# Performance work log

Measured on AMD Instinct MI355X. Metric: run time of the kernel, lower is better.

The kernel has to match this reference:

```python
import jax, jax.numpy as jnp
import numpy as np

B, GRID, CIN, COUT, TDIM, NMODES = 32, 128, 32, 32, 256, 32
M = NMODES // 2 + 1  # kept modes per axis = 17
FFT_NORM = 'forward'


def setup_inputs() -> dict:
    key = jax.random.key(0)
    ks = jax.random.split(key, 10)
    w_std = float(np.sqrt(1.0 / (2.0 * CIN)))          # normal_initializer(in_co_dim)
    k_std = float(np.sqrt(1.0 / TDIM))                 # ~lecun_normal for Dense kernels
    wshape = (M, M, CIN, COUT)
    return {
        'x': jax.random.normal(ks[0], (B, GRID, GRID, CIN), jnp.float32),
        't_emb': jax.random.normal(ks[1], (B, TDIM), jnp.float32),
        'w1_real': w_std * jax.random.normal(ks[2], wshape, jnp.float32),
        'w1_imag': w_std * jax.random.normal(ks[3], wshape, jnp.float32),
        'w2_real': w_std * jax.random.normal(ks[4], wshape, jnp.float32),
        'w2_imag': w_std * jax.random.normal(ks[5], wshape, jnp.float32),
        'k1_real': k_std * jax.random.normal(ks[6], (TDIM, M), jnp.float32),
        'k1_imag': k_std * jax.random.normal(ks[7], (TDIM, M), jnp.float32),
        'k2_real': k_std * jax.random.normal(ks[8], (TDIM, M), jnp.float32),
        'k2_imag': k_std * jax.random.normal(ks[9], (TDIM, M), jnp.float32),
    }


def reference(x, t_emb, w1_real, w1_imag, w2_real, w2_imag,
              k1_real, k1_imag, k2_real, k2_imag):
    b, n = x.shape[0], x.shape[1]
    # rFFT2 over spatial axes: (b, n, n//2+1, cin) complex
    x_ft = jnp.fft.rfft2(x, axes=(1, 2), norm=FFT_NORM)

    w1 = w1_real + 1j * w1_imag  # (M, M, cin, cout)
    w2 = w2_real + 1j * w2_imag
    # Time modulation: Dense(no bias) -> complex per-mode scale t[b, i].
    # The original builds diag(t) and einsums it into the weights; that equals a
    # simple broadcast scale over the first mode axis, fused here.
    t1 = (t_emb @ k1_real) + 1j * (t_emb @ k1_imag)  # (b, M)
    t2 = (t_emb @ k2_real) + 1j * (t_emb @ k2_imag)

    # Mode-truncated complex channel contraction, scaled by t along axis i.
    xf1 = jnp.einsum('bijc,ijco->bijo', x_ft[:, :M, :M, :], w1) * t1[:, :, None, None]
    xf2 = jnp.einsum('bijc,ijco->bijo', x_ft[:, -M:, :M, :], w2) * t2[:, :, None, None]

    out_ft = jnp.zeros((b, n, n // 2 + 1, COUT), dtype=jnp.complex64)
    out_ft = out_ft.at[:, :M, :M, :].set(xf1)
    out_ft = out_ft.at[:, -M:, :M, :].set(xf2)

    return jnp.fft.irfft2(out_ft, s=(n, n), axes=(1, 2), norm=FFT_NORM)
```

## Files before the change

### kernel.cpp

```cpp
#include <hip/hip_runtime.h>
#include <stdint.h>


#define TWO_PI_OVER_128 0.04908738521234052f

__device__ __forceinline__ float4 f4add(float4 a, float4 b) {
    return make_float4(a.x + b.x, a.y + b.y, a.z + b.z, a.w + b.w);
}
__device__ __forceinline__ float4 f4sub(float4 a, float4 b) {
    return make_float4(a.x - b.x, a.y - b.y, a.z - b.z, a.w - b.w);
}

__global__ __launch_bounds__(128) void k_tproj(
    const float* __restrict__ temb, const float* __restrict__ k1r, const float* __restrict__ k1i,
    const float* __restrict__ k2r, const float* __restrict__ k2i, float* __restrict__ tbuf)
{
    int b = blockIdx.x, tid = threadIdx.x;
    __shared__ float ts[256];
    for (int d = tid; d < 256; d += 128) ts[d] = temb[b * 256 + d];
    __syncthreads();
    if (tid < 68) {
        int which = (tid >= 34) ? 1 : 0;
        int rem = tid - which * 34;
        int i = rem >> 1, part = rem & 1;
        const float* kp = which ? (part ? k2i : k2r) : (part ? k1i : k1r);
        float a0 = 0.f, a1 = 0.f, a2 = 0.f, a3 = 0.f;
        for (int d = 0; d < 256; d += 4) {
            a0 = fmaf(ts[d],     kp[(d)     * 17 + i], a0);
            a1 = fmaf(ts[d + 1], kp[(d + 1) * 17 + i], a1);
            a2 = fmaf(ts[d + 2], kp[(d + 2) * 17 + i], a2);
            a3 = fmaf(ts[d + 3], kp[(d + 3) * 17 + i], a3);
        }
        tbuf[((which * 32 + b) * 17 + i) * 2 + part] = (a0 + a1) + (a2 + a3);
    }
}

__global__ __launch_bounds__(64) void k_fwd_y(const float* __restrict__ x, float2* __restrict__ T1)
{
    int blk = blockIdx.x;
    int b = blk >> 7, xr = blk & 127;
    __shared__ float xs[128 * 32];
    __shared__ float2 cst[128];
    int tid = threadIdx.x;
    {
        float s0, c0; sincosf(TWO_PI_OVER_128 * (float)tid, &s0, &c0);
        cst[tid] = make_float2(c0, -s0);
        float s1, c1; sincosf(TWO_PI_OVER_128 * (float)(tid + 64), &s1, &c1);
        cst[tid + 64] = make_float2(c1, -s1);
    }
    const float4* xv = (const float4*)(x + ((size_t)blk << 12));
    float4* xs4 = (float4*)xs;
#pragma unroll
    for (int i = 0; i < 16; ++i) xs4[tid + (i << 6)] = xv[tid + (i << 6)];
    __syncthreads();
    for (int i = tid; i < 1024; i += 64) {
        int c = i & 31, t = i >> 5;
        if (t < 31) {
            int y = t + 1;
            float a  = xs[(y << 5) + c],        bb = xs[((64 - y) << 5) + c];
            float cc = xs[((64 + y) << 5) + c], d  = xs[((128 - y) << 5) + c];
            float Sy = a + d, Dy = a - d, Sm = bb + cc, Dm = bb - cc;
            xs[(y << 5) + c]         = Sy + Sm;
            xs[((64 - y) << 5) + c]  = Sy - Sm;
            xs[((128 - y) << 5) + c] = Dy - Dm;
            xs[((64 + y) << 5) + c]  = Dy + Dm;
        } else {
            float a = xs[(32 << 5) + c], q = xs[(96 << 5) + c];
            xs[(32 << 5) + c] = a + q;
            xs[(96 << 5) + c] = a - q;
        }
    }
    __syncthreads();
    int jg = tid >> 3, cg = tid & 7, c0 = cg << 2;
    int p = jg & 1;
    float re[2][4] = {{0,0,0,0},{0,0,0,0}}, im[2][4] = {{0,0,0,0},{0,0,0,0}};
    int j0 = jg, j1 = jg + 8;
    int idx0 = 0, idx1 = 0;
    for (int y = 1; y <= 31; ++y) {
        idx0 = (idx0 + j0) & 127;
        idx1 = (idx1 + j1) & 127;
        float2 w0 = cst[idx0], w1 = cst[idx1];
        int sr = p ? (64 - y) : y;
        int dr = p ? (64 + y) : (128 - y);
        float4 s = *(const float4*)&xs[(sr << 5) + c0];
        float4 d = *(const float4*)&xs[(dr << 5) + c0];
        re[0][0] = fmaf(s.x, w0.x, re[0][0]);
        re[0][1] = fmaf(s.y, w0.x, re[0][1]);
        re[0][2] = fmaf(s.z, w0.x, re[0][2]);
        re[0][3] = fmaf(s.w, w0.x, re[0][3]);
        im[0][0] = fmaf(d.x, w0.y, im[0][0]);
        im[0][1] = fmaf(d.y, w0.y, im[0][1]);
        im[0][2] = fmaf(d.z, w0.y, im[0][2]);
        im[0][3] = fmaf(d.w, w0.y, im[0][3]);
        re[1][0] = fmaf(s.x, w1.x, re[1][0]);
        re[1][1] = fmaf(s.y, w1.x, re[1][1]);
        re[1][2] = fmaf(s.z, w1.x, re[1][2]);
        re[1][3] = fmaf(s.w, w1.x, re[1][3]);
        im[1][0] = fmaf(d.x, w1.y, im[1][0]);
        im[1][1] = fmaf(d.y, w1.y, im[1][1]);
        im[1][2] = fmaf(d.z, w1.y, im[1][2]);
        im[1][3] = fmaf(d.w, w1.y, im[1][3]);
    }
    const float s_ = 1.f / 16384.f;
    float x0[4], x64[4], S32v[4], D32v[4];
    *(float4*)x0   = *(const float4*)&xs[c0];
    *(float4*)x64  = *(const float4*)&xs[(64 << 5) + c0];
    *(float4*)S32v = *(const float4*)&xs[(32 << 5) + c0];
    *(float4*)D32v = *(const float4*)&xs[(96 << 5) + c0];
    float2 w32 = cst[(j0 << 5) & 127];
    float sg = p ? -1.f : 1.f;
#pragma unroll
    for (int t = 0; t < 2; ++t) {
        int j = jg + t * 8;
        float2* pp = T1 + (((size_t)(b * 17 + j) * 128 + xr) << 5) + c0;
        float4 v0 = make_float4((re[t][0] + x0[0] + sg * x64[0] + S32v[0] * w32.x) * s_,
                                (im[t][0] + D32v[0] * w32.y) * s_,
                                (re[t][1] + x0[1] + sg * x64[1] + S32v[1] * w32.x) * s_,
                                (im[t][1] + D32v[1] * w32.y) * s_);
        float4 v1 = make_float4((re[t][2] + x0[2] + sg * x64[2] + S32v[2] * w32.x) * s_,
                                (im[t][2] + D32v[2] * w32.y) * s_,
                                (re[t][3] + x0[3] + sg * x64[3] + S32v[3] * w32.x) * s_,
                                (im[t][3] + D32v[3] * w32.y) * s_);
        ((float4*)pp)[0] = v0; ((float4*)pp)[1] = v1;
    }
    {
        float re2[4] = {0,0,0,0}, im2[4] = {0,0,0,0};
        float2 w16 = cst[(16 * (jg + 1)) & 127];
        for (int y = jg + 1; y <= 31; y += 8) {
            float4 s = *(const float4*)&xs[(y << 5) + c0];
            float4 d = *(const float4*)&xs[((128 - y) << 5) + c0];
            re2[0] = fmaf(s.x, w16.x, re2[0]); re2[1] = fmaf(s.y, w16.x, re2[1]);
            re2[2] = fmaf(s.z, w16.x, re2[2]); re2[3] = fmaf(s.w, w16.x, re2[3]);
            im2[0] = fmaf(d.x, w16.y, im2[0]); im2[1] = fmaf(d.y, w16.y, im2[1]);
            im2[2] = fmaf(d.z, w16.y, im2[2]); im2[3] = fmaf(d.w, w16.y, im2[3]);
        }
#pragma unroll
        for (int t = 0; t < 4; ++t) {
            re2[t] += __shfl_xor(re2[t], 8);
            re2[t] += __shfl_xor(re2[t], 16);
            re2[t] += __shfl_xor(re2[t], 32);
            im2[t] += __shfl_xor(im2[t], 8);
            im2[t] += __shfl_xor(im2[t], 16);
            im2[t] += __shfl_xor(im2[t], 32);
        }
        if (jg == 0) {
            float2* pp = T1 + (((size_t)(b * 17 + 16) * 128 + xr) << 5) + c0;
            float4 v0 = make_float4((re2[0] + x0[0] + x64[0] + S32v[0]) * s_, im2[0] * s_,
                                    (re2[1] + x0[1] + x64[1] + S32v[1]) * s_, im2[1] * s_);
            float4 v1 = make_float4((re2[2] + x0[2] + x64[2] + S32v[2]) * s_, im2[2] * s_,
                                    (re2[3] + x0[3] + x64[3] + S32v[3]) * s_, im2[3] * s_);
            ((float4*)pp)[0] = v0; ((float4*)pp)[1] = v1;
        }
    }
}

#define XFS 34
__global__ __launch_bounds__(512) void k_mid_fused(
    const float2* __restrict__ T1, const float* __restrict__ w1r, const float* __restrict__ w1i,
    const float* __restrict__ w2r, const float* __restrict__ w2i,
    const float* __restrict__ temb, const float* __restrict__ k1r, const float* __restrict__ k1i,
    const float* __restrict__ k2r, const float* __restrict__ k2i, float2* __restrict__ U)
{
    int blk = blockIdx.x;
    int b = blk / 17, j = blk - b * 17;
    __shared__ float4 Ts4[2048];
    __shared__ float2 Xf[34 * XFS];
    __shared__ float2 cst[128];
    __shared__ float tl[68];
    int tid = threadIdx.x;
    const float4* s4 = (const float4*)(T1 + (size_t)blk * 4096);
    for (int i = tid; i < 2048; i += 512) Ts4[i] = s4[i];
    if (tid < 128) {
        float s, c; sincosf(TWO_PI_OVER_128 * (float)tid, &s, &c);
        cst[tid] = make_float2(c, s);
    }
    __syncthreads();
    {
        int t = tid >> 4, cp = tid & 15;
        if (t < 31) {
            int y = t + 1;
            float4 a  = Ts4[(y << 4) + cp],        bb = Ts4[((64 - y) << 4) + cp];
            float4 cc = Ts4[((64 + y) << 4) + cp], d  = Ts4[((128 - y) << 4) + cp];
            float4 Sy = f4add(a, d), Dy = f4sub(a, d);
            float4 Sm = f4add(bb, cc), Dm = f4sub(bb, cc);
            Ts4[(y << 4) + cp]         = f4add(Sy, Sm);
            Ts4[((64 - y) << 4) + cp]  = f4sub(Sy, Sm);
            Ts4[((128 - y) << 4) + cp] = f4sub(Dy, Dm);
            Ts4[((64 + y) << 4) + cp]  = f4add(Dy, Dm);
        } else {
            float4 a = Ts4[(32 << 4) + cp], q = Ts4[(96 << 4) + cp];
            Ts4[(32 << 4) + cp] = f4add(a, q);
            Ts4[(96 << 4) + cp] = f4sub(a, q);
        }
    }
    __syncthreads();
    if (tid < 288) {
        int cp = tid & 15, u = tid >> 4;
        int f = (u < 16) ? (u + 1) : ((u == 16) ? 0 : 111);
        int p = f & 1;
        float4 t0 = Ts4[cp], t64 = Ts4[(64 << 4) + cp];
        float P0=0,Q0=0,R0=0,T0=0,P1=0,Q1=0,R1=0,T1a=0;
        int idx = 0;
        for (int xx = 1; xx <= 31; ++xx) {
            idx = (idx + f) & 127;
            float2 w = cst[idx];
            float4 S = Ts4[((p ? (64 - xx) : xx) << 4) + cp];
            float4 D = Ts4[((p ? (64 + xx) : (128 - xx)) << 4) + cp];
            P0 = fmaf(S.x, w.x, P0); Q0 = fmaf(D.y, w.y, Q0);
            R0 = fmaf(S.y, w.x, R0); T0 = fmaf(D.x, w.y, T0);
            P1 = fmaf(S.z, w.x, P1); Q1 = fmaf(D.w, w.y, Q1);
            R1 = fmaf(S.w, w.x, R1); T1a = fmaf(D.z, w.y, T1a);
        }
        {
            float2 w32 = cst[(f << 5) & 127];
            float4 S32 = Ts4[(32 << 4) + cp], D32 = Ts4[(96 << 4) + cp];
            P0 = fmaf(S32.x, w32.x, P0); Q0 = fmaf(D32.y, w32.y, Q0);
            R0 = fmaf(S32.y, w32.x, R0); T0 = fmaf(D32.x, w32.y, T0);
            P1 = fmaf(S32.z, w32.x, P1); Q1 = fmaf(D32.w, w32.y, Q1);
            R1 = fmaf(S32.w, w32.x, R1); T1a = fmaf(D32.z, w32.y, T1a);
        }
        float sg = p ? -1.f : 1.f;
        float b0r = t0.x + sg * t64.x, b0i = t0.y + sg * t64.y;
        float b1r = t0.z + sg * t64.z, b1i = t0.w + sg * t64.w;
        int ia = (u == 16) ? 0 : ((u == 17) ? 17 : f);
        Xf[ia * XFS + cp*2]   = make_float2(P0 + Q0 + b0r, R0 - T0 + b0i);
        Xf[ia * XFS + cp*2+1] = make_float2(P1 + Q1 + b1r, R1 - T1a + b1i);
        if (u < 16) {
            int ib = 34 - f;
            Xf[ib * XFS + cp*2]   = make_float2(P0 - Q0 + b0r, R0 + T0 + b0i);
            Xf[ib * XFS + cp*2+1] = make_float2(P1 - Q1 + b1r, R1 + T1a + b1i);
        }
    } else if (tid >= 320 && tid < 388) {
        int r = tid - 320;
        int which = (r >= 34) ? 1 : 0;
        int rem = r - which * 34;
        int i = rem >> 1, part = rem & 1;
        const float* kp = which ? (part ? k2i : k2r) : (part ? k1i : k1r);
        const float* tb = temb + b * 256;
        float a0 = 0.f, a1 = 0.f, a2 = 0.f, a3 = 0.f;
        for (int d = 0; d < 256; d += 4) {
            a0 = fmaf(tb[d],     kp[(d)     * 17 + i], a0);
            a1 = fmaf(tb[d + 1], kp[(d + 1) * 17 + i], a1);
            a2 = fmaf(tb[d + 2], kp[(d + 2) * 17 + i], a2);
            a3 = fmaf(tb[d + 3], kp[(d + 3) * 17 + i], a3);
        }
        tl[which * 34 + (i << 1) + part] = (a0 + a1) + (a2 + a3);
    }
    __syncthreads();
    float2* Ys = (float2*)Ts4;
    if (tid < 272) {
        int oq = tid & 7, ii = tid >> 3;
        int o0 = oq << 2;
        int irow = (ii < 17) ? ii : ii - 17;
        const float* wr = ((ii < 17) ? w1r : w2r) + ((irow * 17 + j) << 10) + o0;
        const float* wi = ((ii < 17) ? w1i : w2i) + ((irow * 17 + j) << 10) + o0;
        float ar0=0,ai0=0,ar1=0,ai1=0,ar2=0,ai2=0,ar3=0,ai3=0;
#pragma unroll 4
        for (int c = 0; c < 32; ++c) {
            float2 xv = Xf[ii * XFS + c];
            float4 wre = *(const float4*)(wr + (c << 5));
            float4 wim = *(const float4*)(wi + (c << 5));
            ar0 = fmaf(xv.x, wre.x, ar0); ar0 = fmaf(-xv.y, wim.x, ar0);
            ai0 = fmaf(xv.x, wim.x, ai0); ai0 = fmaf( xv.y, wre.x, ai0);
            ar1 = fmaf(xv.x, wre.y, ar1); ar1 = fmaf(-xv.y, wim.y, ar1);
            ai1 = fmaf(xv.x, wim.y, ai1); ai1 = fmaf( xv.y, wre.y, ai1);
            ar2 = fmaf(xv.x, wre.z, ar2); ar2 = fmaf(-xv.y, wim.z, ar2);
            ai2 = fmaf(xv.x, wim.z, ai2); ai2 = fmaf( xv.y, wre.z, ai2);
            ar3 = fmaf(xv.x, wre.w, ar3); ar3 = fmaf(-xv.y, wim.w, ar3);
            ai3 = fmaf(xv.x, wim.w, ai3); ai3 = fmaf( xv.y, wre.w, ai3);
        }
        int which = (ii >= 17) ? 1 : 0;
        float tr = tl[which * 34 + (irow << 1)], ti = tl[which * 34 + (irow << 1) + 1];
        float2* yp = Ys + ii * 32 + o0;
        float4 y01 = make_float4(ar0 * tr - ai0 * ti, ar0 * ti + ai0 * tr,
                                 ar1 * tr - ai1 * ti, ar1 * ti + ai1 * tr);
        float4 y23 = make_float4(ar2 * tr - ai2 * ti, ar2 * ti + ai2 * tr,
                                 ar3 * tr - ai3 * ti, ar3 * ti + ai3 * tr);
        ((float4*)yp)[0] = y01;
        ((float4*)yp)[1] = y23;
    }
    __syncthreads();
    {
        int o = tid & 31, g = tid >> 5;
        float yr[34], yi[34];
#pragma unroll
        for (int i = 0; i < 34; ++i) { float2 v = Ys[i * 32 + o]; yr[i] = v.x; yi[i] = v.y; }
        float2* Ub = U + ((size_t)b * 128 * 17 + j) * 32 + o;
        if (g == 0) {
            float sr = 0.f, si = 0.f;
#pragma unroll
            for (int i = 0; i < 34; ++i) { sr += yr[i]; si += yi[i]; }
            Ub[0] = make_float2(sr, si);
        }
        if (g == 1) {
            float sr = 0.f, si = 0.f;
#pragma unroll
            for (int i = 0; i < 34; ++i) {
                float sg2 = (i & 1) ? -1.f : 1.f;
                sr = fmaf(sg2, yr[i], sr); si = fmaf(sg2, yi[i], si);
            }
            Ub[(size_t)64 * 544] = make_float2(sr, si);
        }
        for (int k = 0; k < 2; ++k) {
            int x = 1 + g + (k << 4);
            float A1e=0,A1o=0,A2e=0,A2o=0,A3e=0,A3o=0,A4e=0,A4o=0;
            int idx = 0;
#pragma unroll
            for (int i = 0; i < 17; ++i) {
                float2 w = cst[idx];
                if (i & 1) {
                    A1o = fmaf(yr[i], w.x, A1o); A4o = fmaf(yr[i], w.y, A4o);
                    A3o = fmaf(yi[i], w.x, A3o); A2o = fmaf(yi[i], w.y, A2o);
                } else {
                    A1e = fmaf(yr[i], w.x, A1e); A4e = fmaf(yr[i], w.y, A4e);
                    A3e = fmaf(yi[i], w.x, A3e); A2e = fmaf(yi[i], w.y, A2e);
                }
                idx = (idx + x) & 127;
            }
            idx = (111 * x) & 127;
#pragma unroll
            for (int i = 17; i < 34; ++i) {
                float2 w = cst[idx];
                if (i & 1) {
                    A1o = fmaf(yr[i], w.x, A1o); A4o = fmaf(yr[i], w.y, A4o);
                    A3o = fmaf(yi[i], w.x, A3o); A2o = fmaf(yi[i], w.y, A2o);
                } else {
                    A1e = fmaf(yr[i], w.x, A1e); A4e = fmaf(yr[i], w.y, A4e);
                    A3e = fmaf(yi[i], w.x, A3e); A2e = fmaf(yi[i], w.y, A2e);
                }
                idx = (idx + x) & 127;
            }
            float A1 = A1e + A1o, A2 = A2e + A2o, A3 = A3e + A3o, A4 = A4e + A4o;
            float E1 = A1e - A1o, E2 = A2o - A2e, E3 = A3e - A3o, E4 = A4o - A4e;
            Ub[(size_t)x * 544]         = make_float2(A1 - A2, A3 + A4);
            Ub[(size_t)(128 - x) * 544] = make_float2(A1 + A2, A3 - A4);
            Ub[(size_t)(64 - x) * 544]  = make_float2(E1 - E2, E3 + E4);
            Ub[(size_t)(64 + x) * 544]  = make_float2(E1 + E2, E3 - E4);
        }
    }
}

__global__ __launch_bounds__(256) void k_fwd_x_mix(
    const float2* __restrict__ T1, const float* __restrict__ w1r, const float* __restrict__ w1i,
    const float* __restrict__ w2r, const float* __restrict__ w2i,
    const float* __restrict__ tbuf, float2* __restrict__ Y)
{
    int blk = blockIdx.x;
    int b = blk / 17, j = blk - b * 17;
    __shared__ float4 Ts4[2048];
    __shared__ float2 Xf[34 * 32];
    int tid = threadIdx.x;
    const float4* s4 = (const float4*)(T1 + (size_t)blk * 4096);
    for (int i = tid; i < 2048; i += 256) Ts4[i] = s4[i];
    __syncthreads();
    {
        int cp = tid & 15, g = tid >> 4;
        int il[3] = {g, g + 16, g + 32};
        float stc[3], sts[3];
#pragma unroll
        for (int t = 0; t < 3; ++t) {
            int i = il[t];
            int f = (i < 17) ? i : i + 94;
            float a = -TWO_PI_OVER_128 * (float)(f & 127);
            sincosf(a, &sts[t], &stc[t]);
        }
        float cr[3] = {1.f, 1.f, 1.f}, ci[3] = {0.f, 0.f, 0.f};
        float r0[3] = {0,0,0}, i0[3] = {0,0,0}, r1[3] = {0,0,0}, i1[3] = {0,0,0};
        const float4* Tc = Ts4 + cp;
#pragma unroll 2
        for (int xx = 0; xx < 128; ++xx) {
            float4 tv = Tc[xx << 4];
#pragma unroll
            for (int t = 0; t < 3; ++t) {
                r0[t] += tv.x * cr[t] - tv.y * ci[t];
                i0[t] += tv.x * ci[t] + tv.y * cr[t];
                r1[t] += tv.z * cr[t] - tv.w * ci[t];
                i1[t] += tv.z * ci[t] + tv.w * cr[t];
                float nr = cr[t] * stc[t] - ci[t] * sts[t];
                ci[t] = fmaf(cr[t], sts[t], ci[t] * stc[t]);
                cr[t] = nr;
            }
        }
#pragma unroll
        for (int t = 0; t < 3; ++t) {
            int i = il[t];
            if (i < 34) {
                Xf[i * 32 + cp * 2]     = make_float2(r0[t], i0[t]);
// ... 76 lines not shown

__global__ __launch_bounds__(128) void k_inv_y(const float2* __restrict__ U, float* __restrict__ out)
{
    int blk = blockIdx.x;
    __shared__ float2 Us[17 * 32];
    __shared__ float2 cst[128];
    int tid = threadIdx.x;
    {
        float s, c; sincosf(TWO_PI_OVER_128 * (float)tid, &s, &c);
        cst[tid] = make_float2(c, s);
    }
    const float4* src4 = (const float4*)(U + (size_t)blk * 544);
    float4* Us4 = (float4*)Us;
    for (int i = tid; i < 272; i += 128) Us4[i] = src4[i];
    __syncthreads();
    int cg = tid & 15, yg = tid >> 4, c0 = cg << 1;
    float base0, base1;
    {
        float4 v = *(const float4*)&Us[c0];
        base0 = v.x; base1 = v.z;
    }
    float urr[16][2], uii[16][2];
#pragma unroll
    for (int jj = 1; jj <= 16; ++jj) {
        float4 v = *(const float4*)&Us[jj * 32 + c0];
        urr[jj-1][0] = 2.f * v.x; uii[jj-1][0] = 2.f * v.y;
        urr[jj-1][1] = 2.f * v.z; uii[jj-1][1] = 2.f * v.w;
    }
    float* op = out + ((size_t)blk << 12);
    for (int k = 0; k < 4; ++k) {
        int y = 1 + yg + (k << 3);
        float Ae0=0,Ao0=0,Be0=0,Bo0=0,Ae1=0,Ao1=0,Be1=0,Bo1=0;
        int idx = y;
#pragma unroll
        for (int jj = 0; jj < 16; ++jj) {
            float2 w = cst[idx];
            if (jj & 1) {
                Ae0 = fmaf(urr[jj][0], w.x, Ae0); Be0 = fmaf(uii[jj][0], w.y, Be0);
                Ae1 = fmaf(urr[jj][1], w.x, Ae1); Be1 = fmaf(uii[jj][1], w.y, Be1);
            } else {
                Ao0 = fmaf(urr[jj][0], w.x, Ao0); Bo0 = fmaf(uii[jj][0], w.y, Bo0);
                Ao1 = fmaf(urr[jj][1], w.x, Ao1); Bo1 = fmaf(uii[jj][1], w.y, Bo1);
            }
            idx = (idx + y) & 127;
        }
        float s0 = Ae0 + Ao0, d0 = Be0 + Bo0, e0 = Ae0 - Ao0, f0 = Be0 - Bo0;
        float s1 = Ae1 + Ao1, d1 = Be1 + Bo1, e1 = Ae1 - Ao1, f1 = Be1 - Bo1;
        *(float2*)&op[(y << 5) + c0]         = make_float2(base0 + s0 - d0, base1 + s1 - d1);
        *(float2*)&op[((128 - y) << 5) + c0] = make_float2(base0 + s0 + d0, base1 + s1 + d1);
        *(float2*)&op[((64 - y) << 5) + c0]  = make_float2(base0 + e0 + f0, base1 + e1 + f1);
        *(float2*)&op[((64 + y) << 5) + c0]  = make_float2(base0 + e0 - f0, base1 + e1 - f1);
    }
    if (yg == 0) {
        float s0 = 0.f, s1 = 0.f, a0 = 0.f, a1 = 0.f;
#pragma unroll
        for (int jj = 0; jj < 16; ++jj) {
            s0 += urr[jj][0]; s1 += urr[jj][1];
            float sg = (jj & 1) ? 1.f : -1.f;
            a0 = fmaf(sg, urr[jj][0], a0); a1 = fmaf(sg, urr[jj][1], a1);
        }
        *(float2*)&op[c0]             = make_float2(base0 + s0, base1 + s1);
        *(float2*)&op[(64 << 5) + c0] = make_float2(base0 + a0, base1 + a1);
    }
}

extern "C" void kernel_launch(void* const* d_in, const int* in_sizes, int n_in,
                              void* d_out, int out_size, void* d_ws, size_t ws_size,
                              hipStream_t stream)
{
    const float* x    = (const float*)d_in[0];
    const float* temb = (const float*)d_in[1];
    const float* w1r  = (const float*)d_in[2];
    const float* w1i  = (const float*)d_in[3];
    const float* w2r  = (const float*)d_in[4];
    const float* w2i  = (const float*)d_in[5];
    const float* k1r  = (const float*)d_in[6];
    const float* k1i  = (const float*)d_in[7];
    const float* k2r  = (const float*)d_in[8];
    const float* k2i  = (const float*)d_in[9];
    float* out = (float*)d_out;

    char* ws = (char*)d_ws;
    const size_t T1_BYTES = 17825792;
    const size_t NEED_FUSED = 2 * T1_BYTES + 8704;

    if (ws_size >= NEED_FUSED) {
        float2* T1 = (float2*)ws;
        float2* U  = (float2*)(ws + T1_BYTES);
        k_fwd_y    <<<4096, 64,  0, stream>>>(x, T1);
        k_mid_fused<<<544,  512, 0, stream>>>(T1, w1r, w1i, w2r, w2i,
                                              temb, k1r, k1i, k2r, k2i, U);
        k_inv_y    <<<4096, 128, 0, stream>>>(U, out);
    } else {
        float2* T1 = (float2*)ws;
        float2* Yb = (float2*)(ws + T1_BYTES);
        float*  tb = (float*)(ws + T1_BYTES + 4734976);
        float2* U  = T1;
        k_tproj    <<<32,   128, 0, stream>>>(temb, k1r, k1i, k2r, k2i, tb);
        k_fwd_y    <<<4096, 64,  0, stream>>>(x, T1);
        k_fwd_x_mix<<<544,  256, 0, stream>>>(T1, w1r, w1i, w2r, w2i, tb, Yb);
        k_inv_x    <<<544,  256, 0, stream>>>(Yb, U);
        k_inv_y    <<<4096, 128, 0, stream>>>(U, out);
    }
}
```

Baseline: 183.1 us.

## Split fused mid kernel into forward-x and mix/inverse-x kernels, drop LDS staging in fwd_y

k_fwd_y no longer stages each row in shared memory. It reads the four folded rows straight from global memory and applies the butterfly fold in registers, with two x-rows per 128-thread block. The former 544-block fused middle kernel becomes two kernels of 1088 blocks each: a forward x-DFT split by mode parity that writes truncated modes to a new global buffer and computes the time projection, then a channel mix plus inverse x-DFT split by output-channel half. This raises parallelism and lowers per-block shared memory. The cost is an extra launch, an extra global round trip for the truncated modes, and redundant global loads in fwd_y.

```diff
diff --git a/kernel.cpp b/kernel.cpp
--- a/kernel.cpp
+++ b/kernel.cpp
@@ -35,44 +35,23 @@
     }
 }
 
-__global__ __launch_bounds__(64) void k_fwd_y(const float* __restrict__ x, float2* __restrict__ T1)
+__global__ __launch_bounds__(128) void k_fwd_y(const float* __restrict__ x, float2* __restrict__ T1)
 {
     int blk = blockIdx.x;
-    int b = blk >> 7, xr = blk & 127;
-    __shared__ float xs[128 * 32];
     __shared__ float2 cst[128];
     int tid = threadIdx.x;
-    {
+    if (tid < 128) {
         float s0, c0; sincosf(TWO_PI_OVER_128 * (float)tid, &s0, &c0);
         cst[tid] = make_float2(c0, -s0);
-        float s1, c1; sincosf(TWO_PI_OVER_128 * (float)(tid + 64), &s1, &c1);
-        cst[tid + 64] = make_float2(c1, -s1);
-    }
-    const float4* xv = (const float4*)(x + ((size_t)blk << 12));
-    float4* xs4 = (float4*)xs;
-#pragma unroll
-    for (int i = 0; i < 16; ++i) xs4[tid + (i << 6)] = xv[tid + (i << 6)];
-    __syncthreads();
-    for (int i = tid; i < 1024; i += 64) {
-        int c = i & 31, t = i >> 5;
-        if (t < 31) {
-            int y = t + 1;
-            float a  = xs[(y << 5) + c],        bb = xs[((64 - y) << 5) + c];
-            float cc = xs[((64 + y) << 5) + c], d  = xs[((128 - y) << 5) + c];
-            float Sy = a + d, Dy = a - d, Sm = bb + cc, Dm = bb - cc;
-            xs[(y << 5) + c]         = Sy + Sm;
-            xs[((64 - y) << 5) + c]  = Sy - Sm;
-            xs[((128 - y) << 5) + c] = Dy - Dm;
-            xs[((64 + y) << 5) + c]  = Dy + Dm;
-        } else {
-            float a = xs[(32 << 5) + c], q = xs[(96 << 5) + c];
-            xs[(32 << 5) + c] = a + q;
-            xs[(96 << 5) + c] = a - q;
-        }
-    }
-    __syncthreads();
-    int jg = tid >> 3, cg = tid & 7, c0 = cg << 2;
+    }
+    __syncthreads();
+    int half = tid >> 6, t64i = tid & 63;
+    int b = blk >> 6, xp = blk & 63;
+    int xr = (xp << 1) + half;
+    const float* W = x + (((size_t)(b * 128 + xr)) << 12);
+    int jg = t64i >> 3, cg = t64i & 7, c0 = cg << 2;
     int p = jg & 1;
+    float sfold = p ? -1.f : 1.f;
     float re[2][4] = {{0,0,0,0},{0,0,0,0}}, im[2][4] = {{0,0,0,0},{0,0,0,0}};
     int j0 = jg, j1 = jg + 8;
     int idx0 = 0, idx1 = 0;
@@ -80,59 +59,71 @@
         idx0 = (idx0 + j0) & 127;
         idx1 = (idx1 + j1) & 127;
         float2 w0 = cst[idx0], w1 = cst[idx1];
-        int sr = p ? (64 - y) : y;
-        int dr = p ? (64 + y) : (128 - y);
-        float4 s = *(const float4*)&xs[(sr << 5) + c0];
-        float4 d = *(const float4*)&xs[(dr << 5) + c0];
+        float4 a  = *(const float4*)&W[(y << 5) + c0];
+        float4 d  = *(const float4*)&W[((128 - y) << 5) + c0];
+        float4 bb = *(const float4*)&W[((64 - y) << 5) + c0];
+        float4 cc = *(const float4*)&W[((64 + y) << 5) + c0];
+        float4 Sy = f4add(a, d), Dy = f4sub(a, d);
+        float4 Sm = f4add(bb, cc), Dm = f4sub(bb, cc);
+        float4 s = make_float4(fmaf(sfold, Sm.x, Sy.x), fmaf(sfold, Sm.y, Sy.y),
+                               fmaf(sfold, Sm.z, Sy.z), fmaf(sfold, Sm.w, Sy.w));
+        float4 dd = make_float4(fmaf(-sfold, Dm.x, Dy.x), fmaf(-sfold, Dm.y, Dy.y),
+                                fmaf(-sfold, Dm.z, Dy.z), fmaf(-sfold, Dm.w, Dy.w));
         re[0][0] = fmaf(s.x, w0.x, re[0][0]);
         re[0][1] = fmaf(s.y, w0.x, re[0][1]);
         re[0][2] = fmaf(s.z, w0.x, re[0][2]);
         re[0][3] = fmaf(s.w, w0.x, re[0][3]);
-        im[0][0] = fmaf(d.x, w0.y, im[0][0]);
-        im[0][1] = fmaf(d.y, w0.y, im[0][1]);
-        im[0][2] = fmaf(d.z, w0.y, im[0][2]);
-        im[0][3] = fmaf(d.w, w0.y, im[0][3]);
+        im[0][0] = fmaf(dd.x, w0.y, im[0][0]);
+        im[0][1] = fmaf(dd.y, w0.y, im[0][1]);
+        im[0][2] = fmaf(dd.z, w0.y, im[0][2]);
+        im[0][3] = fmaf(dd.w, w0.y, im[0][3]);
         re[1][0] = fmaf(s.x, w1.x, re[1][0]);
         re[1][1] = fmaf(s.y, w1.x, re[1][1]);
         re[1][2] = fmaf(s.z, w1.x, re[1][2]);
         re[1][3] = fmaf(s.w, w1.x, re[1][3]);
-        im[1][0] = fmaf(d.x, w1.y, im[1][0]);
-        im[1][1] = fmaf(d.y, w1.y, im[1][1]);
-        im[1][2] = fmaf(d.z, w1.y, im[1][2]);
-        im[1][3] = fmaf(d.w, w1.y, im[1][3]);
+        im[1][0] = fmaf(dd.x, w1.y, im[1][0]);
+        im[1][1] = fmaf(dd.y, w1.y, im[1][1]);
+        im[1][2] = fmaf(dd.z, w1.y, im[1][2]);
+        im[1][3] = fmaf(dd.w, w1.y, im[1][3]);
     }
     const float s_ = 1.f / 16384.f;
-    float x0[4], x64[4], S32v[4], D32v[4];
-    *(float4*)x0   = *(const float4*)&xs[c0];
-    *(float4*)x64  = *(const float4*)&xs[(64 << 5) + c0];
-    *(float4*)S32v = *(const float4*)&xs[(32 << 5) + c0];
-    *(float4*)D32v = *(const float4*)&xs[(96 << 5) + c0];
+    float4 x0  = *(const float4*)&W[c0];
+    float4 x64 = *(const float4*)&W[(64 << 5) + c0];
+    float4 r32 = *(const float4*)&W[(32 << 5) + c0];
+    float4 r96 = *(const float4*)&W[(96 << 5) + c0];
+    float4 S32 = f4add(r32, r96), D32 = f4sub(r32, r96);
     float2 w32 = cst[(j0 << 5) & 127];
+    float x0a[4], x64a[4], S32a[4], D32a[4];
+    *(float4*)x0a = x0; *(float4*)x64a = x64; *(float4*)S32a = S32; *(float4*)D32a = D32;
     float sg = p ? -1.f : 1.f;
 #pragma unroll
     for (int t = 0; t < 2; ++t) {
         int j = jg + t * 8;
         float2* pp = T1 + (((size_t)(b * 17 + j) * 128 + xr) << 5) + c0;
-        float4 v0 = make_float4((re[t][0] + x0[0] + sg * x64[0] + S32v[0] * w32.x) * s_,
-                                (im[t][0] + D32v[0] * w32.y) * s_,
-                                (re[t][1] + x0[1] + sg * x64[1] + S32v[1] * w32.x) * s_,
-                                (im[t][1] + D32v[1] * w32.y) * s_);
-        float4 v1 = make_float4((re[t][2] + x0[2] + sg * x64[2] + S32v[2] * w32.x) * s_,
-                                (im[t][2] + D32v[2] * w32.y) * s_,
-                                (re[t][3] + x0[3] + sg * x64[3] + S32v[3] * w32.x) * s_,
-                                (im[t][3] + D32v[3] * w32.y) * s_);
+        float4 v0 = make_float4((re[t][0] + x0a[0] + sg * x64a[0] + S32a[0] * w32.x) * s_,
+                                (im[t][0] + D32a[0] * w32.y) * s_,
+                                (re[t][1] + x0a[1] + sg * x64a[1] + S32a[1] * w32.x) * s_,
+                                (im[t][1] + D32a[1] * w32.y) * s_);
+        float4 v1 = make_float4((re[t][2] + x0a[2] + sg * x64a[2] + S32a[2] * w32.x) * s_,
+                                (im[t][2] + D32a[2] * w32.y) * s_,
+                                (re[t][3] + x0a[3] + sg * x64a[3] + S32a[3] * w32.x) * s_,
+                                (im[t][3] + D32a[3] * w32.y) * s_);
         ((float4*)pp)[0] = v0; ((float4*)pp)[1] = v1;
     }
     {
         float re2[4] = {0,0,0,0}, im2[4] = {0,0,0,0};
         float2 w16 = cst[(16 * (jg + 1)) & 127];
         for (int y = jg + 1; y <= 31; y += 8) {
-            float4 s = *(const float4*)&xs[(y << 5) + c0];
-            float4 d = *(const float4*)&xs[((128 - y) << 5) + c0];
+            float4 a  = *(const float4*)&W[(y << 5) + c0];
+            float4 d  = *(const float4*)&W[((128 - y) << 5) + c0];
+            float4 bb = *(const float4*)&W[((64 - y) << 5) + c0];
+            float4 cc = *(const float4*)&W[((64 + y) << 5) + c0];
+            float4 s  = f4add(f4add(a, d), f4add(bb, cc));
+            float4 dd = f4sub(f4sub(a, d), f4sub(bb, cc));
             re2[0] = fmaf(s.x, w16.x, re2[0]); re2[1] = fmaf(s.y, w16.x, re2[1]);
             re2[2] = fmaf(s.z, w16.x, re2[2]); re2[3] = fmaf(s.w, w16.x, re2[3]);
-            im2[0] = fmaf(d.x, w16.y, im2[0]); im2[1] = fmaf(d.y, w16.y, im2[1]);
-            im2[2] = fmaf(d.z, w16.y, im2[2]); im2[3] = fmaf(d.w, w16.y, im2[3]);
+            im2[0] = fmaf(dd.x, w16.y, im2[0]); im2[1] = fmaf(dd.y, w16.y, im2[1]);
+            im2[2] = fmaf(dd.z, w16.y, im2[2]); im2[3] = fmaf(dd.w, w16.y, im2[3]);
         }
 #pragma unroll
         for (int t = 0; t < 4; ++t) {
@@ -145,67 +136,70 @@
         }
         if (jg == 0) {
             float2* pp = T1 + (((size_t)(b * 17 + 16) * 128 + xr) << 5) + c0;
-            float4 v0 = make_float4((re2[0] + x0[0] + x64[0] + S32v[0]) * s_, im2[0] * s_,
-                                    (re2[1] + x0[1] + x64[1] + S32v[1]) * s_, im2[1] * s_);
-            float4 v1 = make_float4((re2[2] + x0[2] + x64[2] + S32v[2]) * s_, im2[2] * s_,
-                                    (re2[3] + x0[3] + x64[3] + S32v[3]) * s_, im2[3] * s_);
+            float4 v0 = make_float4((re2[0] + x0a[0] + x64a[0] + S32a[0]) * s_, im2[0] * s_,
+                                    (re2[1] + x0a[1] + x64a[1] + S32a[1]) * s_, im2[1] * s_);
+            float4 v1 = make_float4((re2[2] + x0a[2] + x64a[2] + S32a[2]) * s_, im2[2] * s_,
+                                    (re2[3] + x0a[3] + x64a[3] + S32a[3]) * s_, im2[3] * s_);
             ((float4*)pp)[0] = v0; ((float4*)pp)[1] = v1;
         }
     }
 }
 
-#define XFS 34
-__global__ __launch_bounds__(512) void k_mid_fused(
-    const float2* __restrict__ T1, const float* __restrict__ w1r, const float* __restrict__ w1i,
-    const float* __restrict__ w2r, const float* __restrict__ w2i,
-    const float* __restrict__ temb, const float* __restrict__ k1r, const float* __restrict__ k1i,
-    const float* __restrict__ k2r, const float* __restrict__ k2i, float2* __restrict__ U)
+__global__ __launch_bounds__(256) void k_fwd_x(
+    const float2* __restrict__ T1, const float* __restrict__ temb,
+    const float* __restrict__ k1r, const float* __restrict__ k1i,
+    const float* __restrict__ k2r, const float* __restrict__ k2i,
+    float2* __restrict__ Xfg, float* __restrict__ tbuf)
 {
     int blk = blockIdx.x;
-    int b = blk / 17, j = blk - b * 17;
-    __shared__ float4 Ts4[2048];
-    __shared__ float2 Xf[34 * XFS];
+    int b = blk / 34, r = blk - b * 34;
+    int j = r >> 1, par = r & 1;
+    __shared__ float4 FH[65 * 16];
     __shared__ float2 cst[128];
-    __shared__ float tl[68];
     int tid = threadIdx.x;
-    const float4* s4 = (const float4*)(T1 + (size_t)blk * 4096);
-    for (int i = tid; i < 2048; i += 512) Ts4[i] = s4[i];
     if (tid < 128) {
         float s, c; sincosf(TWO_PI_OVER_128 * (float)tid, &s, &c);
         cst[tid] = make_float2(c, s);
     }
-    __syncthreads();
-    {
-        int t = tid >> 4, cp = tid & 15;
-        if (t < 31) {
-            int y = t + 1;
-            float4 a  = Ts4[(y << 4) + cp],        bb = Ts4[((64 - y) << 4) + cp];
-            float4 cc = Ts4[((64 + y) << 4) + cp], d  = Ts4[((128 - y) << 4) + cp];
+    const float4* T = (const float4*)(T1 + (size_t)(b * 17 + j) * 4096);
+    float sfold = par ? -1.f : 1.f;
+    for (int i = tid; i < 544; i += 256) {
+        if (i < 496) {
+            int y = (i >> 4) + 1, cp = i & 15;
+            float4 a  = T[(y << 4) + cp];
+            float4 d  = T[((128 - y) << 4) + cp];
+            float4 bb = T[((64 - y) << 4) + cp];
+            float4 cc = T[((64 + y) << 4) + cp];
             float4 Sy = f4add(a, d), Dy = f4sub(a, d);
             float4 Sm = f4add(bb, cc), Dm = f4sub(bb, cc);
-            Ts4[(y << 4) + cp]         = f4add(Sy, Sm);
-            Ts4[((64 - y) << 4) + cp]  = f4sub(Sy, Sm);
-            Ts4[((128 - y) << 4) + cp] = f4sub(Dy, Dm);
-            Ts4[((64 + y) << 4) + cp]  = f4add(Dy, Dm);
+            FH[((y - 1) << 4) + cp] = make_float4(
+                fmaf(sfold, Sm.x, Sy.x), fmaf(sfold, Sm.y, Sy.y),
+                fmaf(sfold, Sm.z, Sy.z), fmaf(sfold, Sm.w, Sy.w));
+            FH[((30 + y) << 4) + cp] = make_float4(
+                fmaf(-sfold, Dm.x, Dy.x), fmaf(-sfold, Dm.y, Dy.y),
+                fmaf(-sfold, Dm.z, Dy.z), fmaf(-sfold, Dm.w, Dy.w));
+        } else if (i < 512) {
+            int cp = i - 496;
+            float4 s32 = T[(32 << 4) + cp], s96 = T[(96 << 4) + cp];
+            FH[(62 << 4) + cp] = par ? f4sub(s32, s96) : f4add(s32, s96);
         } else {
-            float4 a = Ts4[(32 << 4) + cp], q = Ts4[(96 << 4) + cp];
-            Ts4[(32 << 4) + cp] = f4add(a, q);
-            Ts4[(96 << 4) + cp] = f4sub(a, q);
-        }
-    }
-    __syncthreads();
-    if (tid < 288) {
+            int k = i - 512, cp = k & 15;
+            if (k < 16) FH[(63 << 4) + cp] = T[cp];
+            else        FH[(64 << 4) + cp] = T[(64 << 4) + cp];
+        }
+    }
+    __syncthreads();
+    if (tid < 144) {
         int cp = tid & 15, u = tid >> 4;
-        int f = (u < 16) ? (u + 1) : ((u == 16) ? 0 : 111);
-        int p = f & 1;
-        float4 t0 = Ts4[cp], t64 = Ts4[(64 << 4) + cp];
+        int f = par ? ((u < 8) ? (2 * u + 1) : 111)
+                    : ((u < 8) ? (2 * u + 2) : 0);
         float P0=0,Q0=0,R0=0,T0=0,P1=0,Q1=0,R1=0,T1a=0;
         int idx = 0;
         for (int xx = 1; xx <= 31; ++xx) {
             idx = (idx + f) & 127;
             float2 w = cst[idx];
-            float4 S = Ts4[((p ? (64 - xx) : xx) << 4) + cp];
-            float4 D = Ts4[((p ? (64 + xx) : (128 - xx)) << 4) + cp];
+            float4 S = FH[((xx - 1) << 4) + cp];
+            float4 D = FH[((30 + xx) << 4) + cp];
             P0 = fmaf(S.x, w.x, P0); Q0 = fmaf(D.y, w.y, Q0);
             R0 = fmaf(S.y, w.x, R0); T0 = fmaf(D.x, w.y, T0);
             P1 = fmaf(S.z, w.x, P1); Q1 = fmaf(D.w, w.y, Q1);
@@ -213,27 +207,34 @@
         }
         {
             float2 w32 = cst[(f << 5) & 127];
-            float4 S32 = Ts4[(32 << 4) + cp], D32 = Ts4[(96 << 4) + cp];
-            P0 = fmaf(S32.x, w32.x, P0); Q0 = fmaf(D32.y, w32.y, Q0);
-            R0 = fmaf(S32.y, w32.x, R0); T0 = fmaf(D32.x, w32.y, T0);
-            P1 = fmaf(S32.z, w32.x, P1); Q1 = fmaf(D32.w, w32.y, Q1);
-            R1 = fmaf(S32.w, w32.x, R1); T1a = fmaf(D32.z, w32.y, T1a);
-        }
-        float sg = p ? -1.f : 1.f;
+            float4 SD = FH[(62 << 4) + cp];
+            if (par == 0) {
+                P0 = fmaf(SD.x, w32.x, P0); R0 = fmaf(SD.y, w32.x, R0);
+                P1 = fmaf(SD.z, w32.x, P1); R1 = fmaf(SD.w, w32.x, R1);
+            } else {
+                Q0 = fmaf(SD.y, w32.y, Q0); T0 = fmaf(SD.x, w32.y, T0);
+                Q1 = fmaf(SD.w, w32.y, Q1); T1a = fmaf(SD.z, w32.y, T1a);
+            }
+        }
+        float4 t0 = FH[(63 << 4) + cp], t64 = FH[(64 << 4) + cp];
+        float sg = par ? -1.f : 1.f;
         float b0r = t0.x + sg * t64.x, b0i = t0.y + sg * t64.y;
         float b1r = t0.z + sg * t64.z, b1i = t0.w + sg * t64.w;
-        int ia = (u == 16) ? 0 : ((u == 17) ? 17 : f);
-        Xf[ia * XFS + cp*2]   = make_float2(P0 + Q0 + b0r, R0 - T0 + b0i);
-        Xf[ia * XFS + cp*2+1] = make_float2(P1 + Q1 + b1r, R1 - T1a + b1i);
-        if (u < 16) {
+        int ia = (u == 8) ? (par ? 17 : 0) : f;
+        size_t tile = (size_t)(b * 17 + j) * 34;
+        float4* Xa = (float4*)(Xfg + (tile + ia) * 32 + cp * 2);
+        Xa[0] = make_float4(P0 + Q0 + b0r, R0 - T0 + b0i,
+                            P1 + Q1 + b1r, R1 - T1a + b1i);
+        if (u < 8) {
             int ib = 34 - f;
-            Xf[ib * XFS + cp*2]   = make_float2(P0 - Q0 + b0r, R0 + T0 + b0i);
-            Xf[ib * XFS + cp*2+1] = make_float2(P1 - Q1 + b1r, R1 + T1a + b1i);
-        }
-    } else if (tid >= 320 && tid < 388) {
-        int r = tid - 320;
-        int which = (r >= 34) ? 1 : 0;
-        int rem = r - which * 34;
+            float4* Xb = (float4*)(Xfg + (tile + ib) * 32 + cp * 2);
+            Xb[0] = make_float4(P0 - Q0 + b0r, R0 + T0 + b0i,
+                                P1 - Q1 + b1r, R1 + T1a + b1i);
+        }
+    } else if (par == 0 && tid >= 160 && tid < 228) {
+        int rr = tid - 160;
+        int which = (rr >= 34) ? 1 : 0;
+        int rem = rr - which * 34;
         int i = rem >> 1, part = rem & 1;
         const float* kp = which ? (part ? k2i : k2r) : (part ? k1i : k1r);
         const float* tb = temb + b * 256;
@@ -244,20 +245,42 @@
             a2 = fmaf(tb[d + 2], kp[(d + 2) * 17 + i], a2);
             a3 = fmaf(tb[d + 3], kp[(d + 3) * 17 + i], a3);
         }
-        tl[which * 34 + (i << 1) + part] = (a0 + a1) + (a2 + a3);
-    }
-    __syncthreads();
-    float2* Ys = (float2*)Ts4;
-    if (tid < 272) {
-        int oq = tid & 7, ii = tid >> 3;
-        int o0 = oq << 2;
+        tbuf[((which * 32 + b) * 17 + i) * 2 + part] = (a0 + a1) + (a2 + a3);
+    }
+}
+
+__global__ __launch_bounds__(256) void k_mix_inv_x(
+    const float2* __restrict__ Xfg, const float* __restrict__ w1r, const float* __restrict__ w1i,
+    const float* __restrict__ w2r, const float* __restrict__ w2i,
+    const float* __restrict__ tbuf, float2* __restrict__ U)
+{
+    int blk = blockIdx.x;
+    int b = blk / 34, r = blk - b * 34;
+    int j = r >> 1, oh = r & 1;
+    __shared__ float2 Xb[34 * 34];
+    __shared__ float2 Ys[34 * 18];
+    __shared__ float2 cst[128];
+    int tid = threadIdx.x;
+    if (tid < 128) {
+        float s, c; sincosf(TWO_PI_OVER_128 * (float)tid, &s, &c);
+        cst[tid] = make_float2(c, s);
+    }
+    const float4* X4 = (const float4*)(Xfg + (size_t)(b * 17 + j) * 34 * 32);
+    for (int i = tid; i < 544; i += 256) {
+        int row = i >> 4, cp = i & 15;
+        *(float4*)&Xb[row * 34 + (cp << 1)] = X4[(row << 4) + cp];
+    }
+    __syncthreads();
+    if (tid < 136) {
+        int oq = tid & 3, ii = tid >> 2;
+        int o0 = (oh << 4) + (oq << 2);
         int irow = (ii < 17) ? ii : ii - 17;
         const float* wr = ((ii < 17) ? w1r : w2r) + ((irow * 17 + j) << 10) + o0;
         const float* wi = ((ii < 17) ? w1i : w2i) + ((irow * 17 + j) << 10) + o0;
         float ar0=0,ai0=0,ar1=0,ai1=0,ar2=0,ai2=0,ar3=0,ai3=0;
 #pragma unroll 4
         for (int c = 0; c < 32; ++c) {
-            float2 xv = Xf[ii * XFS + c];
+            float2 xv = Xb[ii * 34 + c];
             float4 wre = *(const float4*)(wr + (c << 5));
             float4 wim = *(const float4*)(wi + (c << 5));
             ar0 = fmaf(xv.x, wre.x, ar0); ar0 = fmaf(-xv.y, wim.x, ar0);
@@ -270,21 +293,21 @@
             ai3 = fmaf(xv.x, wim.w, ai3); ai3 = fmaf( xv.y, wre.w, ai3);
         }
         int which = (ii >= 17) ? 1 : 0;
-        float tr = tl[which * 34 + (irow << 1)], ti = tl[which * 34 + (irow << 1) + 1];
-        float2* yp = Ys + ii * 32 + o0;
-        float4 y01 = make_float4(ar0 * tr - ai0 * ti, ar0 * ti + ai0 * tr,
-                                 ar1 * tr - ai1 * ti, ar1 * ti + ai1 * tr);
-        float4 y23 = make_float4(ar2 * tr - ai2 * ti, ar2 * ti + ai2 * tr,
-                                 ar3 * tr - ai3 * ti, ar3 * ti + ai3 * tr);
-        ((float4*)yp)[0] = y01;
-        ((float4*)yp)[1] = y23;
+        const float* tp = tbuf + ((which * 32 + b) * 17 + irow) * 2;
+        float tr = tp[0], ti = tp[1];
+        float2* yp = Ys + ii * 18 + (oq << 2);
+        ((float4*)yp)[0] = make_float4(ar0 * tr - ai0 * ti, ar0 * ti + ai0 * tr,
+                                       ar1 * tr - ai1 * ti, ar1 * ti + ai1 * tr);
+        ((float4*)yp)[1] = make_float4(ar2 * tr - ai2 * ti, ar2 * ti + ai2 * tr,
+                                       ar3 * tr - ai3 * ti, ar3 * ti + ai3 * tr);
     }
     __syncthreads();
     {
-        int o = tid & 31, g = tid >> 5;
+        int ol = tid & 15, g = tid >> 4;
+        int o = (oh << 4) + ol;
         float yr[34], yi[34];
 #pragma unroll
-        for (int i = 0; i < 34; ++i) { float2 v = Ys[i * 32 + o]; yr[i] = v.x; yi[i] = v.y; }
+        for (int i = 0; i < 34; ++i) { float2 v = Ys[i * 18 + ol]; yr[i] = v.x; yi[i] = v.y; }
         float2* Ub = U + ((size_t)b * 128 * 17 + j) * 32 + o;
         if (g == 0) {
             float sr = 0.f, si = 0.f;
@@ -545,22 +568,25 @@
 
     char* ws = (char*)d_ws;
     const size_t T1_BYTES = 17825792;
-    const size_t NEED_FUSED = 2 * T1_BYTES + 8704;
-
-    if (ws_size >= NEED_FUSED) {
-        float2* T1 = (float2*)ws;
-        float2* U  = (float2*)(ws + T1_BYTES);
-        k_fwd_y    <<<4096, 64,  0, stream>>>(x, T1);
-        k_mid_fused<<<544,  512, 0, stream>>>(T1, w1r, w1i, w2r, w2i,
-                                              temb, k1r, k1i, k2r, k2i, U);
+    const size_t XF_BYTES = 4734976;
+    const size_t NEED_NEW = 2 * T1_BYTES + XF_BYTES + 8704;
+
+    if (ws_size >= NEED_NEW) {
+        float2* T1  = (float2*)ws;
+        float2* U   = (float2*)(ws + T1_BYTES);
+        float2* Xfg = (float2*)(ws + 2 * T1_BYTES);
+        float*  tb  = (float*)(ws + 2 * T1_BYTES + XF_BYTES);
+        k_fwd_y    <<<2048, 128, 0, stream>>>(x, T1);
+        k_fwd_x    <<<1088, 256, 0, stream>>>(T1, temb, k1r, k1i, k2r, k2i, Xfg, tb);
+        k_mix_inv_x<<<1088, 256, 0, stream>>>(Xfg, w1r, w1i, w2r, w2i, tb, U);
         k_inv_y    <<<4096, 128, 0, stream>>>(U, out);
     } else {
         float2* T1 = (float2*)ws;
         float2* Yb = (float2*)(ws + T1_BYTES);
-        float*  tb = (float*)(ws + T1_BYTES + 4734976);
+        float*  tb = (float*)(ws + T1_BYTES + XF_BYTES);
         float2* U  = T1;
         k_tproj    <<<32,   128, 0, stream>>>(temb, k1r, k1i, k2r, k2i, tb);
-        k_fwd_y    <<<4096, 64,  0, stream>>>(x, T1);
+        k_fwd_y    <<<2048, 128, 0, stream>>>(x, T1);
         k_fwd_x_mix<<<544,  256, 0, stream>>>(T1, w1r, w1i, w2r, w2i, tb, Yb);
         k_inv_x    <<<544,  256, 0, stream>>>(Yb, U);
         k_inv_y    <<<4096, 128, 0, stream>>>(U, out);
```

Result: slower. 213.5 us (+16.6%).

## Widen forward-y FFT blocks and split mid kernel across output-channel halves

Applied to the files above, without the earlier changes.

The forward y-axis DFT kernel now uses 128 threads per block, so each thread computes one output frequency instead of two. The fused mid kernel is split so each block handles half of the output channels, doubling the grid from 544 to 1088 blocks. Each thread's inverse-x work drops from two x values to one. The aim is more parallelism and occupancy on a GPU with many CUs, in exchange for loading each T1 slab twice and repeating the forward-x transform and time projection in both halves.

```diff
diff --git a/kernel.cpp b/kernel.cpp
--- a/kernel.cpp
+++ b/kernel.cpp
@@ -35,7 +35,7 @@
     }
 }
 
-__global__ __launch_bounds__(64) void k_fwd_y(const float* __restrict__ x, float2* __restrict__ T1)
+__global__ __launch_bounds__(128) void k_fwd_y(const float* __restrict__ x, float2* __restrict__ T1)
 {
     int blk = blockIdx.x;
     int b = blk >> 7, xr = blk & 127;
@@ -45,15 +45,13 @@
     {
         float s0, c0; sincosf(TWO_PI_OVER_128 * (float)tid, &s0, &c0);
         cst[tid] = make_float2(c0, -s0);
-        float s1, c1; sincosf(TWO_PI_OVER_128 * (float)(tid + 64), &s1, &c1);
-        cst[tid + 64] = make_float2(c1, -s1);
     }
     const float4* xv = (const float4*)(x + ((size_t)blk << 12));
     float4* xs4 = (float4*)xs;
 #pragma unroll
-    for (int i = 0; i < 16; ++i) xs4[tid + (i << 6)] = xv[tid + (i << 6)];
-    __syncthreads();
-    for (int i = tid; i < 1024; i += 64) {
+    for (int i = 0; i < 8; ++i) xs4[tid + (i << 7)] = xv[tid + (i << 7)];
+    __syncthreads();
+    for (int i = tid; i < 1024; i += 128) {
         int c = i & 31, t = i >> 5;
         if (t < 31) {
             int y = t + 1;
@@ -73,33 +71,23 @@
     __syncthreads();
     int jg = tid >> 3, cg = tid & 7, c0 = cg << 2;
     int p = jg & 1;
-    float re[2][4] = {{0,0,0,0},{0,0,0,0}}, im[2][4] = {{0,0,0,0},{0,0,0,0}};
-    int j0 = jg, j1 = jg + 8;
-    int idx0 = 0, idx1 = 0;
+    float re[4] = {0,0,0,0}, im[4] = {0,0,0,0};
+    int idx0 = 0;
     for (int y = 1; y <= 31; ++y) {
-        idx0 = (idx0 + j0) & 127;
-        idx1 = (idx1 + j1) & 127;
-        float2 w0 = cst[idx0], w1 = cst[idx1];
+        idx0 = (idx0 + jg) & 127;
+        float2 w0 = cst[idx0];
         int sr = p ? (64 - y) : y;
         int dr = p ? (64 + y) : (128 - y);
         float4 s = *(const float4*)&xs[(sr << 5) + c0];
         float4 d = *(const float4*)&xs[(dr << 5) + c0];
-        re[0][0] = fmaf(s.x, w0.x, re[0][0]);
-        re[0][1] = fmaf(s.y, w0.x, re[0][1]);
-        re[0][2] = fmaf(s.z, w0.x, re[0][2]);
-        re[0][3] = fmaf(s.w, w0.x, re[0][3]);
-        im[0][0] = fmaf(d.x, w0.y, im[0][0]);
-        im[0][1] = fmaf(d.y, w0.y, im[0][1]);
-        im[0][2] = fmaf(d.z, w0.y, im[0][2]);
-        im[0][3] = fmaf(d.w, w0.y, im[0][3]);
-        re[1][0] = fmaf(s.x, w1.x, re[1][0]);
-        re[1][1] = fmaf(s.y, w1.x, re[1][1]);
-        re[1][2] = fmaf(s.z, w1.x, re[1][2]);
-        re[1][3] = fmaf(s.w, w1.x, re[1][3]);
-        im[1][0] = fmaf(d.x, w1.y, im[1][0]);
-        im[1][1] = fmaf(d.y, w1.y, im[1][1]);
-        im[1][2] = fmaf(d.z, w1.y, im[1][2]);
-        im[1][3] = fmaf(d.w, w1.y, im[1][3]);
+        re[0] = fmaf(s.x, w0.x, re[0]);
+        re[1] = fmaf(s.y, w0.x, re[1]);
+        re[2] = fmaf(s.z, w0.x, re[2]);
+        re[3] = fmaf(s.w, w0.x, re[3]);
+        im[0] = fmaf(d.x, w0.y, im[0]);
+        im[1] = fmaf(d.y, w0.y, im[1]);
+        im[2] = fmaf(d.z, w0.y, im[2]);
+        im[3] = fmaf(d.w, w0.y, im[3]);
     }
     const float s_ = 1.f / 16384.f;
     float x0[4], x64[4], S32v[4], D32v[4];
@@ -107,26 +95,25 @@
     *(float4*)x64  = *(const float4*)&xs[(64 << 5) + c0];
     *(float4*)S32v = *(const float4*)&xs[(32 << 5) + c0];
     *(float4*)D32v = *(const float4*)&xs[(96 << 5) + c0];
-    float2 w32 = cst[(j0 << 5) & 127];
+    float2 w32 = cst[(jg << 5) & 127];
     float sg = p ? -1.f : 1.f;
-#pragma unroll
-    for (int t = 0; t < 2; ++t) {
-        int j = jg + t * 8;
-        float2* pp = T1 + (((size_t)(b * 17 + j) * 128 + xr) << 5) + c0;
-        float4 v0 = make_float4((re[t][0] + x0[0] + sg * x64[0] + S32v[0] * w32.x) * s_,
-                                (im[t][0] + D32v[0] * w32.y) * s_,
-                                (re[t][1] + x0[1] + sg * x64[1] + S32v[1] * w32.x) * s_,
-                                (im[t][1] + D32v[1] * w32.y) * s_);
-        float4 v1 = make_float4((re[t][2] + x0[2] + sg * x64[2] + S32v[2] * w32.x) * s_,
-                                (im[t][2] + D32v[2] * w32.y) * s_,
-                                (re[t][3] + x0[3] + sg * x64[3] + S32v[3] * w32.x) * s_,
-                                (im[t][3] + D32v[3] * w32.y) * s_);
+    {
+        float2* pp = T1 + (((size_t)(b * 17 + jg) * 128 + xr) << 5) + c0;
+        float4 v0 = make_float4((re[0] + x0[0] + sg * x64[0] + S32v[0] * w32.x) * s_,
+                                (im[0] + D32v[0] * w32.y) * s_,
+                                (re[1] + x0[1] + sg * x64[1] + S32v[1] * w32.x) * s_,
+                                (im[1] + D32v[1] * w32.y) * s_);
+        float4 v1 = make_float4((re[2] + x0[2] + sg * x64[2] + S32v[2] * w32.x) * s_,
+                                (im[2] + D32v[2] * w32.y) * s_,
+                                (re[3] + x0[3] + sg * x64[3] + S32v[3] * w32.x) * s_,
+                                (im[3] + D32v[3] * w32.y) * s_);
         ((float4*)pp)[0] = v0; ((float4*)pp)[1] = v1;
     }
-    {
+    if (tid < 64) {
         float re2[4] = {0,0,0,0}, im2[4] = {0,0,0,0};
-        float2 w16 = cst[(16 * (jg + 1)) & 127];
-        for (int y = jg + 1; y <= 31; y += 8) {
+        int jg8 = tid >> 3;
+        float2 w16 = cst[(16 * (jg8 + 1)) & 127];
+        for (int y = jg8 + 1; y <= 31; y += 8) {
             float4 s = *(const float4*)&xs[(y << 5) + c0];
             float4 d = *(const float4*)&xs[((128 - y) << 5) + c0];
             re2[0] = fmaf(s.x, w16.x, re2[0]); re2[1] = fmaf(s.y, w16.x, re2[1]);
@@ -143,7 +130,7 @@
             im2[t] += __shfl_xor(im2[t], 16);
             im2[t] += __shfl_xor(im2[t], 32);
         }
-        if (jg == 0) {
+        if (jg8 == 0) {
             float2* pp = T1 + (((size_t)(b * 17 + 16) * 128 + xr) << 5) + c0;
             float4 v0 = make_float4((re2[0] + x0[0] + x64[0] + S32v[0]) * s_, im2[0] * s_,
                                     (re2[1] + x0[1] + x64[1] + S32v[1]) * s_, im2[1] * s_);
@@ -155,20 +142,21 @@
 }
 
 #define XFS 34
-__global__ __launch_bounds__(512) void k_mid_fused(
+__global__ __launch_bounds__(512) void k_mid_half(
     const float2* __restrict__ T1, const float* __restrict__ w1r, const float* __restrict__ w1i,
     const float* __restrict__ w2r, const float* __restrict__ w2i,
     const float* __restrict__ temb, const float* __restrict__ k1r, const float* __restrict__ k1i,
     const float* __restrict__ k2r, const float* __restrict__ k2i, float2* __restrict__ U)
 {
     int blk = blockIdx.x;
-    int b = blk / 17, j = blk - b * 17;
+    int b = blk / 34, r = blk - b * 34;
+    int j = r >> 1, oh = r & 1;
     __shared__ float4 Ts4[2048];
     __shared__ float2 Xf[34 * XFS];
     __shared__ float2 cst[128];
     __shared__ float tl[68];
     int tid = threadIdx.x;
-    const float4* s4 = (const float4*)(T1 + (size_t)blk * 4096);
+    const float4* s4 = (const float4*)(T1 + (size_t)(b * 17 + j) * 4096);
     for (int i = tid; i < 2048; i += 512) Ts4[i] = s4[i];
     if (tid < 128) {
         float s, c; sincosf(TWO_PI_OVER_128 * (float)tid, &s, &c);
@@ -231,9 +219,9 @@
             Xf[ib * XFS + cp*2+1] = make_float2(P1 - Q1 + b1r, R1 + T1a + b1i);
         }
     } else if (tid >= 320 && tid < 388) {
-        int r = tid - 320;
-        int which = (r >= 34) ? 1 : 0;
-        int rem = r - which * 34;
+        int rr = tid - 320;
+        int which = (rr >= 34) ? 1 : 0;
+        int rem = rr - which * 34;
         int i = rem >> 1, part = rem & 1;
         const float* kp = which ? (part ? k2i : k2r) : (part ? k1i : k1r);
         const float* tb = temb + b * 256;
@@ -248,9 +236,9 @@
     }
     __syncthreads();
     float2* Ys = (float2*)Ts4;
-    if (tid < 272) {
-        int oq = tid & 7, ii = tid >> 3;
-        int o0 = oq << 2;
+    if (tid < 136) {
+        int oq = tid & 3, ii = tid >> 2;
+        int o0 = (oh << 4) + (oq << 2);
         int irow = (ii < 17) ? ii : ii - 17;
         const float* wr = ((ii < 17) ? w1r : w2r) + ((irow * 17 + j) << 10) + o0;
         const float* wi = ((ii < 17) ? w1i : w2i) + ((irow * 17 + j) << 10) + o0;
@@ -270,21 +258,21 @@
             ai3 = fmaf(xv.x, wim.w, ai3); ai3 = fmaf( xv.y, wre.w, ai3);
         }
         int which = (ii >= 17) ? 1 : 0;
-        float tr = tl[which * 34 + (irow << 1)], ti = tl[which * 34 + (irow << 1) + 1];
-        float2* yp = Ys + ii * 32 + o0;
-        float4 y01 = make_float4(ar0 * tr - ai0 * ti, ar0 * ti + ai0 * tr,
-                                 ar1 * tr - ai1 * ti, ar1 * ti + ai1 * tr);
-        float4 y23 = make_float4(ar2 * tr - ai2 * ti, ar2 * ti + ai2 * tr,
-                                 ar3 * tr - ai3 * ti, ar3 * ti + ai3 * tr);
-        ((float4*)yp)[0] = y01;
-        ((float4*)yp)[1] = y23;
-    }
-    __syncthreads();
-    {
-        int o = tid & 31, g = tid >> 5;
+        int irow2 = (ii < 17) ? ii : ii - 17;
+        float tr = tl[which * 34 + (irow2 << 1)], ti = tl[which * 34 + (irow2 << 1) + 1];
+        float2* yp = Ys + ii * 16 + (oq << 2);
+        ((float4*)yp)[0] = make_float4(ar0 * tr - ai0 * ti, ar0 * ti + ai0 * tr,
+                                       ar1 * tr - ai1 * ti, ar1 * ti + ai1 * tr);
+        ((float4*)yp)[1] = make_float4(ar2 * tr - ai2 * ti, ar2 * ti + ai2 * tr,
+                                       ar3 * tr - ai3 * ti, ar3 * ti + ai3 * tr);
+    }
+    __syncthreads();
+    {
+        int ol = tid & 15, g = tid >> 4;
+        int o = (oh << 4) + ol;
         float yr[34], yi[34];
 #pragma unroll
-        for (int i = 0; i < 34; ++i) { float2 v = Ys[i * 32 + o]; yr[i] = v.x; yi[i] = v.y; }
+        for (int i = 0; i < 34; ++i) { float2 v = Ys[i * 16 + ol]; yr[i] = v.x; yi[i] = v.y; }
         float2* Ub = U + ((size_t)b * 128 * 17 + j) * 32 + o;
         if (g == 0) {
             float sr = 0.f, si = 0.f;
@@ -301,8 +289,8 @@
             }
             Ub[(size_t)64 * 544] = make_float2(sr, si);
         }
-        for (int k = 0; k < 2; ++k) {
-            int x = 1 + g + (k << 4);
+        {
+            int x = g + 1;
             float A1e=0,A1o=0,A2e=0,A2o=0,A3e=0,A3o=0,A4e=0,A4o=0;
             int idx = 0;
 #pragma unroll
@@ -550,17 +538,17 @@
     if (ws_size >= NEED_FUSED) {
         float2* T1 = (float2*)ws;
         float2* U  = (float2*)(ws + T1_BYTES);
-        k_fwd_y    <<<4096, 64,  0, stream>>>(x, T1);
-        k_mid_fused<<<544,  512, 0, stream>>>(T1, w1r, w1i, w2r, w2i,
-                                              temb, k1r, k1i, k2r, k2i, U);
-        k_inv_y    <<<4096, 128, 0, stream>>>(U, out);
+        k_fwd_y   <<<4096, 128, 0, stream>>>(x, T1);
+        k_mid_half<<<1088, 512, 0, stream>>>(T1, w1r, w1i, w2r, w2i,
+                                             temb, k1r, k1i, k2r, k2i, U);
+        k_inv_y   <<<4096, 128, 0, stream>>>(U, out);
     } else {
         float2* T1 = (float2*)ws;
         float2* Yb = (float2*)(ws + T1_BYTES);
         float*  tb = (float*)(ws + T1_BYTES + 4734976);
         float2* U  = T1;
         k_tproj    <<<32,   128, 0, stream>>>(temb, k1r, k1i, k2r, k2i, tb);
-        k_fwd_y    <<<4096, 64,  0, stream>>>(x, T1);
+        k_fwd_y    <<<4096, 128, 0, stream>>>(x, T1);
         k_fwd_x_mix<<<544,  256, 0, stream>>>(T1, w1r, w1i, w2r, w2i, tb, Yb);
         k_inv_x    <<<544,  256, 0, stream>>>(Yb, U);
         k_inv_y    <<<4096, 128, 0, stream>>>(U, out);
```

Measured after the change: 193.8 us. +5.8%, slower.
